# Kernel optimization log

Hardware: AMD Instinct MI355X
Metric: run time of the kernel (lower is better)

## Reference

```python
import jax, jax.numpy as jnp
import numpy as np


def setup_inputs() -> dict:
    key = jax.random.key(0)
    k1, k2, k3, k4 = jax.random.split(key, 4)
    B, T, C, H = 4, 4096, 1024, 64
    x = jax.random.normal(k1, (B, T, C), dtype=jnp.float32)
    Wq = jax.random.normal(k2, (C, H), dtype=jnp.float32) * (C ** -0.5)
    Wk = jax.random.normal(k3, (C, H), dtype=jnp.float32) * (C ** -0.5)
    Wv = jax.random.normal(k4, (C, H), dtype=jnp.float32) * (C ** -0.5)
    return {"x": x, "Wq": Wq, "Wk": Wk, "Wv": Wv}


def reference(x, Wq, Wk, Wv):
    B, T, C = x.shape
    q = jnp.einsum('btc,ch->bth', x, Wq)  # [B,T,H]
    k = jnp.einsum('btc,ch->bth', x, Wk)
    v = jnp.einsum('btc,ch->bth', x, Wv)
    # NOTE: original scales by C**0.5 (embed_dim), not head_size**0.5
    scale = jnp.asarray(C, x.dtype) ** 0.5
    wei = jnp.einsum('bth,bsh->bts', q, k) / scale  # [B,T,T]
    causal = jnp.tril(jnp.ones((T, T), dtype=bool))
    wei = jnp.where(causal, wei, -jnp.inf)
    wei = jax.nn.softmax(wei, axis=-1)  # dropout p=0.0 -> identity
    return jnp.einsum('bts,bsh->bth', wei, v)  # [B,T,H]
```

## Files before the change

### kernel.cpp

```cpp
#include <hip/hip_runtime.h>
#include <hip/hip_bf16.h>

typedef __bf16 bf16;
typedef __bf16 bf16x8 __attribute__((ext_vector_type(8)));
typedef __bf16 bf16x4 __attribute__((ext_vector_type(4)));
typedef float  f32x4  __attribute__((ext_vector_type(4)));

#define MFMA16(A, B, C) __builtin_amdgcn_mfma_f32_16x16x32_bf16((A), (B), (C), 0, 0, 0)

static constexpr int Bn = 4;
static constexpr int T  = 4096;
static constexpr int Cd = 1024;
static constexpr int H  = 64;
static constexpr int NG = 192;
static constexpr int CH = 8;
static constexpr int SLOTS_PER_B = 288;
static constexpr float QSCALE = 0.045084220f;

__device__ inline void dma16(const void* g, void* l) {
    __builtin_amdgcn_global_load_lds(
        (const __attribute__((address_space(1))) unsigned int*)g,
        (__attribute__((address_space(3))) unsigned int*)l, 16, 0, 0);
}

__device__ __forceinline__ void waitcnt_vm(int n) {
    if (n == 0)      asm volatile("s_waitcnt vmcnt(0)" ::: "memory");
    else if (n == 1) asm volatile("s_waitcnt vmcnt(1)" ::: "memory");
    else             asm volatile("s_waitcnt vmcnt(2)" ::: "memory");
}

__device__ inline bf16x8 cvt_bf16x8(float4 a, float4 b) {
    bf16x8 r;
    r[0] = (bf16)a.x; r[1] = (bf16)a.y; r[2] = (bf16)a.z; r[3] = (bf16)a.w;
    r[4] = (bf16)b.x; r[5] = (bf16)b.y; r[6] = (bf16)b.z; r[7] = (bf16)b.w;
    return r;
}

__global__ __launch_bounds__(256) void wt_kernel(const float* __restrict__ Wq,
                                                 const float* __restrict__ Wk,
                                                 const float* __restrict__ Wv,
                                                 bf16* __restrict__ Wt) {
    __shared__ float s[64][65];
    const int cb = blockIdx.x;
    const int m  = blockIdx.y;
    const float* W = (m == 0) ? Wq : (m == 1) ? Wk : Wv;
    for (int i = threadIdx.x; i < 64 * 64; i += 256) {
        const int c = i >> 6, h = i & 63;
        s[c][h] = W[(cb * 64 + c) * H + h];
    }
    __syncthreads();
    for (int i = threadIdx.x; i < 64 * 64; i += 256) {
        const int n = i >> 6, c = i & 63;
        Wt[(m * 64 + n) * Cd + cb * 64 + c] = (bf16)s[c][n];
    }
}

__global__ __launch_bounds__(512, 4) void proj_kernel(const float* __restrict__ x,
                                                      const bf16* __restrict__ Wt,
                                                      bf16* __restrict__ qw,
                                                      bf16* __restrict__ kw,
                                                      bf16* __restrict__ vtw) {
    const int tid  = threadIdx.x;
    const int lane = tid & 63;
    const int w    = tid >> 6;
    const int wr   = w >> 2;
    const int wc   = w & 3;
    const int ml   = lane & 15;
    const int quad = lane >> 4;

    const long r0 = (long)blockIdx.x * 32;

    __shared__ float sX[4][32][64];
    __shared__ bf16  sW[2][192][64];

    const int xrow = w * 4 + (lane >> 4);
    const float* gx = x + (r0 + xrow) * Cd + (((lane & 15) ^ (xrow & 15)) << 2);
    const int wchunk = ((lane & 7) ^ (lane >> 3)) << 3;
    const bf16* gw0 = Wt + (long)(w * 24 + 0 + (lane >> 3)) * Cd + wchunk;
    const bf16* gw1 = Wt + (long)(w * 24 + 8 + (lane >> 3)) * Cd + wchunk;
    const bf16* gw2 = Wt + (long)(w * 24 + 16 + (lane >> 3)) * Cd + wchunk;

    f32x4 acc[3];
    #pragma unroll
    for (int j = 0; j < 3; ++j) acc[j] = f32x4{0.f, 0.f, 0.f, 0.f};

    dma16(gx, &sX[0][w * 4][0]);
    dma16(gw0, &sW[0][w * 24 + 0][0]);
    dma16(gw1, &sW[0][w * 24 + 8][0]);
    dma16(gw2, &sW[0][w * 24 + 16][0]);
    dma16(gx + 64,  &sX[1][w * 4][0]);
    dma16(gx + 128, &sX[2][w * 4][0]);

    const int arow = wr * 16 + ml;
    const int brow0 = wc * 48 + ml;
    const int bsw = ml & 7;

    #pragma unroll
    for (int t = 0; t < 16; ++t) {
        waitcnt_vm(t == 0 ? 2 : (t <= 13 ? 1 : 0));
        __builtin_amdgcn_sched_barrier(0);
        __builtin_amdgcn_s_barrier();
        __builtin_amdgcn_sched_barrier(0);

        if (t + 1 < 16) {
            dma16(gw0 + (t + 1) * 64, &sW[(t + 1) & 1][w * 24 + 0][0]);
            dma16(gw1 + (t + 1) * 64, &sW[(t + 1) & 1][w * 24 + 8][0]);
            dma16(gw2 + (t + 1) * 64, &sW[(t + 1) & 1][w * 24 + 16][0]);
        }
        if (t + 3 < 16) dma16(gx + (t + 3) * 64, &sX[(t + 3) & 3][w * 4][0]);

        const int bx = t & 3, bw = t & 1;
        __builtin_amdgcn_s_setprio(1);
        #pragma unroll
        for (int ks = 0; ks < 2; ++ks) {
            const int ca = (ks * 8 + quad * 2) ^ ml;
            const float4 lo = *(const float4*)&sX[bx][arow][ca << 2];
            const float4 hi = *(const float4*)&sX[bx][arow][(ca ^ 1) << 2];
            const bf16x8 af = cvt_bf16x8(lo, hi);
            const int cb0 = (ks * 4 + quad) ^ bsw;
            acc[0] = MFMA16(af, *(const bf16x8*)&sW[bw][brow0 + 0][cb0 << 3], acc[0]);
            acc[1] = MFMA16(af, *(const bf16x8*)&sW[bw][brow0 + 16][cb0 << 3], acc[1]);
            acc[2] = MFMA16(af, *(const bf16x8*)&sW[bw][brow0 + 32][cb0 << 3], acc[2]);
        }
        __builtin_amdgcn_s_setprio(0);
    }

    const int b = (int)(r0 >> 12);
    const long rowb = r0 + wr * 16 + quad * 4;
    const int  tloc = (int)(rowb & 4095);

    #pragma unroll
    for (int f = 0; f < 3; ++f) {
        const int base = wc * 48 + f * 16;
        const int sel  = base >> 6;
        const int h    = (base & 63) + ml;
        if (sel == 0) {
            #pragma unroll
            for (int rr = 0; rr < 4; ++rr)
                qw[(rowb + rr) * H + h] = (bf16)(acc[f][rr] * QSCALE);
        } else if (sel == 1) {
            #pragma unroll
            for (int rr = 0; rr < 4; ++rr)
                kw[(rowb + rr) * H + h] = (bf16)acc[f][rr];
        } else {
            bf16x4 pv;
            #pragma unroll
            for (int rr = 0; rr < 4; ++rr) pv[rr] = (bf16)acc[f][rr];
            *(bf16x4*)(vtw + ((long)(b * H + h)) * T + tloc) = pv;
        }
    }
}

__global__ __launch_bounds__(256, 4) void attn_kernel(const bf16* __restrict__ qw,
                                                      const bf16* __restrict__ kw,
                                                      const bf16* __restrict__ vtw,
                                                      float* __restrict__ pO,
                                                      float* __restrict__ pL) {
    const int u = blockIdx.x;
    int g = 0;
    #pragma unroll
    for (int gg = 1; gg < 8; ++gg) if (u >= (gg * (gg + 1)) / 2) g = gg;
    const int c  = u - (g * (g + 1)) / 2;
    const int r  = blockIdx.y;
    const int b  = blockIdx.z;
    const int qt = g * 8 + r;

    const int tid  = threadIdx.x;
    const int lane = tid & 63;
    const int w    = tid >> 6;
    const int ml   = lane & 15;
    const int quad = lane >> 4;
    const int mx   = ml & 7;

    __shared__ bf16 sK[2][64][64];
    __shared__ bf16 sVt[2][64][64];
    __shared__ bf16 sP[4][16][64];

    const int t0 = qt * 64;

    const bf16* q0 = qw + ((long)b * T + t0 + w * 16 + ml) * H;
    const bf16x8 aq0 = *(const bf16x8*)(q0 + quad * 8);
    const bf16x8 aq1 = *(const bf16x8*)(q0 + 32 + quad * 8);

    f32x4 O[4];
    #pragma unroll
    for (int ht = 0; ht < 4; ++ht) O[ht] = f32x4{0.f, 0.f, 0.f, 0.f};
    float lrow[4] = {0.f, 0.f, 0.f, 0.f};

    const int trow = t0 + w * 16 + quad * 4;
    const int jt0 = c * CH;
    const int jt1 = (c == g) ? qt + 1 : (c + 1) * CH;

    const int drow = w * 8 + (lane >> 3);
    const int dsw  = ((lane & 7) ^ (drow & 7)) << 3;
    const bf16* kbase = kw + (long)b * T * H;
    const bf16* vbase = vtw + (long)b * H * T;
    const long koffA = (long)drow * H + dsw;
    const long koffB = koffA + 32 * H;
    const long voffA = (long)drow * T + dsw;
    const long voffB = voffA + (long)32 * T;

    {
        const long ks0 = (long)jt0 * 64;
        dma16(kbase + ks0 * H + koffA, &sK[0][w * 8][0]);
        dma16(kbase + ks0 * H + koffB, &sK[0][32 + w * 8][0]);
        dma16(vbase + ks0 + voffA, &sVt[0][w * 8][0]);
        dma16(vbase + ks0 + voffB, &sVt[0][32 + w * 8][0]);
    }

    int buf = 0;
    for (int jt = jt0; jt < jt1; ++jt) {
        asm volatile("s_waitcnt vmcnt(0)" ::: "memory");
        __builtin_amdgcn_sched_barrier(0);
        __builtin_amdgcn_s_barrier();
        __builtin_amdgcn_sched_barrier(0);

        if (jt + 1 < jt1) {
            const long ksn = (long)(jt + 1) * 64;
            dma16(kbase + ksn * H + koffA, &sK[buf ^ 1][w * 8][0]);
            dma16(kbase + ksn * H + koffB, &sK[buf ^ 1][32 + w * 8][0]);
            dma16(vbase + ksn + voffA, &sVt[buf ^ 1][w * 8][0]);
            dma16(vbase + ksn + voffB, &sVt[buf ^ 1][32 + w * 8][0]);
        }

        const int s0 = jt * 64;
        const bool diag = (jt == qt);
        #pragma unroll
        for (int nt = 0; nt < 4; ++nt) {
            f32x4 sacc = f32x4{0.f, 0.f, 0.f, 0.f};
            __builtin_amdgcn_s_setprio(1);
            sacc = MFMA16(aq0, *(const bf16x8*)&sK[buf][nt * 16 + ml][(quad ^ mx) << 3], sacc);
            sacc = MFMA16(aq1, *(const bf16x8*)&sK[buf][nt * 16 + ml][((4 + quad) ^ mx) << 3], sacc);
            __builtin_amdgcn_s_setprio(0);
            const int col = s0 + nt * 16 + ml;
            #pragma unroll
            for (int rr = 0; rr < 4; ++rr) {
                const float p = (diag && col > trow + rr) ? 0.f : exp2f(sacc[rr]);
                lrow[rr] += p;
                const int row = quad * 4 + rr;
                const int sw  = (row & 7) ^ ((row & 8) >> 2);
                sP[w][row][(((nt * 2 + (ml >> 3)) ^ sw) << 3) | (ml & 7)] = (bf16)p;
            }
        }
        asm volatile("s_waitcnt lgkmcnt(0)" ::: "memory");
        __builtin_amdgcn_sched_barrier(0);

        __builtin_amdgcn_s_setprio(1);
        #pragma unroll
        for (int ks = 0; ks < 2; ++ks) {
            const int pch = ((ks * 4 + quad) ^ (ml & 7) ^ ((ml & 8) >> 2)) << 3;
            const bf16x8 ap = *(const bf16x8*)&sP[w][ml][pch];
            #pragma unroll
            for (int ht = 0; ht < 4; ++ht)
                O[ht] = MFMA16(ap,
                    *(const bf16x8*)&sVt[buf][ht * 16 + ml][(((ks << 2) + quad) ^ mx) << 3],
                    O[ht]);
        }
        __builtin_amdgcn_s_setprio(0);

        buf ^= 1;
    }

    #pragma unroll
    for (int d = 1; d < 16; d <<= 1)
        #pragma unroll
        for (int rr = 0; rr < 4; ++rr)
            lrow[rr] += __shfl_xor(lrow[rr], d, 64);

    const long slot = (long)b * SLOTS_PER_B + (long)(g + 1) * (4 * g + r) + c;
    float* po = pO + slot * 4096 + (w * 16) * 64;
    #pragma unroll
    for (int ht = 0; ht < 4; ++ht)
        #pragma unroll
        for (int rr = 0; rr < 4; ++rr)
            po[(quad * 4 + rr) * 64 + ht * 16 + ml] = O[ht][rr];
    if (ml == 0) {
        #pragma unroll
        for (int rr = 0; rr < 4; ++rr)
            pL[slot * 64 + w * 16 + quad * 4 + rr] = lrow[rr];
    }
}

__global__ __launch_bounds__(256) void combine_kernel(const float* __restrict__ pO,
                                                      const float* __restrict__ pL,
                                                      float* __restrict__ out) {
    const int qt = blockIdx.x;
    const int b  = blockIdx.y;
    const int g  = qt >> 3, r = qt & 7;
    const int nch = g + 1;
    const long slot0 = (long)b * SLOTS_PER_B + (long)(g + 1) * (4 * g + r);

    const int tid = threadIdx.x;
    const int row = tid >> 2;
    const int q4  = tid & 3;

    f32x4 o[4];
    #pragma unroll
    for (int j = 0; j < 4; ++j) o[j] = f32x4{0.f, 0.f, 0.f, 0.f};
    float l = 0.f;

    for (int cc = 0; cc < nch; ++cc) {
        const float* po = pO + (slot0 + cc) * 4096 + row * 64 + q4 * 16;
        #pragma unroll
        for (int j = 0; j < 4; ++j) o[j] += *(const f32x4*)(po + j * 4);
        l += pL[(slot0 + cc) * 64 + row];
    }
    const float inv = 1.f / l;
    float* op = out + ((long)b * T + qt * 64 + row) * H + q4 * 16;
    #pragma unroll
    for (int j = 0; j < 4; ++j) {
        f32x4 v = o[j];
        v[0] *= inv; v[1] *= inv; v[2] *= inv; v[3] *= inv;
        *(f32x4*)(op + j * 4) = v;
    }
}

extern "C" void kernel_launch(void* const* d_in, const int* in_sizes, int n_in,
                              void* d_out, int out_size, void* d_ws, size_t ws_size,
                              hipStream_t stream) {
    const float* x  = (const float*)d_in[0];
    const float* Wq = (const float*)d_in[1];
    const float* Wk = (const float*)d_in[2];
    const float* Wv = (const float*)d_in[3];
    float* out = (float*)d_out;

    char* ws = (char*)d_ws;
    const size_t WT_BYTES = (size_t)NG * Cd * sizeof(bf16);
    const size_t QK_BYTES = (size_t)Bn * T * H * sizeof(bf16);
    const size_t PO_OFF   = WT_BYTES + 3 * QK_BYTES;
    const size_t PO_BYTES = (size_t)Bn * SLOTS_PER_B * 4096 * sizeof(float);
    bf16*  Wt  = (bf16*)ws;
    bf16*  qw  = (bf16*)(ws + WT_BYTES);
    bf16*  kw  = (bf16*)(ws + WT_BYTES + QK_BYTES);
    bf16*  vtw = (bf16*)(ws + WT_BYTES + 2 * QK_BYTES);
    float* pO  = (float*)(ws + PO_OFF);
    float* pL  = (float*)(ws + PO_OFF + PO_BYTES);

    wt_kernel<<<dim3(16, 3), dim3(256), 0, stream>>>(Wq, Wk, Wv, Wt);
    proj_kernel<<<dim3((Bn * T) / 32), dim3(512), 0, stream>>>(x, Wt, qw, kw, vtw);
    attn_kernel<<<dim3(36, CH, Bn), dim3(256), 0, stream>>>(qw, kw, vtw, pO, pL);
    combine_kernel<<<dim3(T / 64, Bn), dim3(256), 0, stream>>>(pO, pL, out);
}
```

Measured before the change: 151.8 us.

## Fuse split-KV combine into attention kernel via last-block atomic counter

```diff
diff --git a/kernel.cpp b/kernel.cpp
--- a/kernel.cpp
+++ b/kernel.cpp
@@ -39,7 +39,9 @@
 __global__ __launch_bounds__(256) void wt_kernel(const float* __restrict__ Wq,
                                                  const float* __restrict__ Wk,
                                                  const float* __restrict__ Wv,
-                                                 bf16* __restrict__ Wt) {
+                                                 bf16* __restrict__ Wt,
+                                                 int* __restrict__ cnt) {
+    if (blockIdx.x == 0 && blockIdx.y == 0) cnt[threadIdx.x] = 0;
     __shared__ float s[64][65];
     const int cb = blockIdx.x;
     const int m  = blockIdx.y;
@@ -155,7 +157,9 @@
                                                       const bf16* __restrict__ kw,
                                                       const bf16* __restrict__ vtw,
                                                       float* __restrict__ pO,
-                                                      float* __restrict__ pL) {
+                                                      float* __restrict__ pL,
+                                                      int* __restrict__ cnt,
+                                                      float* __restrict__ out) {
     const int u = blockIdx.x;
     int g = 0;
     #pragma unroll
@@ -175,6 +179,7 @@
     __shared__ bf16 sK[2][64][64];
     __shared__ bf16 sVt[2][64][64];
     __shared__ bf16 sP[4][16][64];
+    __shared__ int s_old;
 
     const int t0 = qt * 64;
 
@@ -267,7 +272,21 @@
         for (int rr = 0; rr < 4; ++rr)
             lrow[rr] += __shfl_xor(lrow[rr], d, 64);
 
-    const long slot = (long)b * SLOTS_PER_B + (long)(g + 1) * (4 * g + r) + c;
+    if (g == 0) {
+        float inv[4];
+        #pragma unroll
+        for (int rr = 0; rr < 4; ++rr) inv[rr] = 1.f / lrow[rr];
+        float* op = out + ((long)b * T + t0 + w * 16 + quad * 4) * H;
+        #pragma unroll
+        for (int ht = 0; ht < 4; ++ht)
+            #pragma unroll
+            for (int rr = 0; rr < 4; ++rr)
+                op[rr * H + ht * 16 + ml] = O[ht][rr] * inv[rr];
+        return;
+    }
+
+    const long slot0 = (long)b * SLOTS_PER_B + (long)(g + 1) * (4 * g + r);
+    const long slot  = slot0 + c;
     float* po = pO + slot * 4096 + (w * 16) * 64;
     #pragma unroll
     for (int ht = 0; ht < 4; ++ht)
@@ -279,30 +298,23 @@
         for (int rr = 0; rr < 4; ++rr)
             pL[slot * 64 + w * 16 + quad * 4 + rr] = lrow[rr];
     }
-}
-
-__global__ __launch_bounds__(256) void combine_kernel(const float* __restrict__ pO,
-                                                      const float* __restrict__ pL,
-                                                      float* __restrict__ out) {
-    const int qt = blockIdx.x;
-    const int b  = blockIdx.y;
-    const int g  = qt >> 3, r = qt & 7;
-    const int nch = g + 1;
-    const long slot0 = (long)b * SLOTS_PER_B + (long)(g + 1) * (4 * g + r);
-
-    const int tid = threadIdx.x;
+
+    __threadfence();
+    if (tid == 0) s_old = atomicAdd(&cnt[b * 64 + qt], 1);
+    __syncthreads();
+    if (s_old != g) return;
+
+    __threadfence();
     const int row = tid >> 2;
     const int q4  = tid & 3;
-
     f32x4 o[4];
     #pragma unroll
     for (int j = 0; j < 4; ++j) o[j] = f32x4{0.f, 0.f, 0.f, 0.f};
     float l = 0.f;
-
-    for (int cc = 0; cc < nch; ++cc) {
-        const float* po = pO + (slot0 + cc) * 4096 + row * 64 + q4 * 16;
-        #pragma unroll
-        for (int j = 0; j < 4; ++j) o[j] += *(const f32x4*)(po + j * 4);
+    for (int cc = 0; cc <= g; ++cc) {
+        const float* pp = pO + (slot0 + cc) * 4096 + row * 64 + q4 * 16;
+        #pragma unroll
+        for (int j = 0; j < 4; ++j) o[j] += *(const f32x4*)(pp + j * 4);
         l += pL[(slot0 + cc) * 64 + row];
     }
     const float inv = 1.f / l;
@@ -329,15 +341,16 @@
     const size_t QK_BYTES = (size_t)Bn * T * H * sizeof(bf16);
     const size_t PO_OFF   = WT_BYTES + 3 * QK_BYTES;
     const size_t PO_BYTES = (size_t)Bn * SLOTS_PER_B * 4096 * sizeof(float);
+    const size_t PL_BYTES = (size_t)Bn * SLOTS_PER_B * 64 * sizeof(float);
     bf16*  Wt  = (bf16*)ws;
     bf16*  qw  = (bf16*)(ws + WT_BYTES);
     bf16*  kw  = (bf16*)(ws + WT_BYTES + QK_BYTES);
     bf16*  vtw = (bf16*)(ws + WT_BYTES + 2 * QK_BYTES);
     float* pO  = (float*)(ws + PO_OFF);
     float* pL  = (float*)(ws + PO_OFF + PO_BYTES);
-
-    wt_kernel<<<dim3(16, 3), dim3(256), 0, stream>>>(Wq, Wk, Wv, Wt);
+    int*   cnt = (int*)(ws + PO_OFF + PO_BYTES + PL_BYTES);
+
+    wt_kernel<<<dim3(16, 3), dim3(256), 0, stream>>>(Wq, Wk, Wv, Wt, cnt);
     proj_kernel<<<dim3((Bn * T) / 32), dim3(512), 0, stream>>>(x, Wt, qw, kw, vtw);
-    attn_kernel<<<dim3(36, CH, Bn), dim3(256), 0, stream>>>(qw, kw, vtw, pO, pL);
-    combine_kernel<<<dim3(T / 64, Bn), dim3(256), 0, stream>>>(pO, pL, out);
-}
+    attn_kernel<<<dim3(36, CH, Bn), dim3(256), 0, stream>>>(qw, kw, vtw, pO, pL, cnt, out);
+}
```

Result: slower. 343.0 us (+126.0%).
